# Kernel tuning notes

Hardware: AMD Instinct MI355X
Metric: run time of the kernel (lower is better)

## Reference

```python
import jax, jax.numpy as jnp
import numpy as np

B, T, I = 32768, 28, 28
H, C = 128, 10


def setup_inputs() -> dict:
    key = jax.random.key(0)
    ks = jax.random.split(key, 7)
    s_u = 1.0 / np.sqrt(I)
    s_w = 1.0 / np.sqrt(H)
    return {
        "x": jax.random.normal(ks[0], (B, T, I), dtype=jnp.float32),
        "U_w": jax.random.uniform(ks[1], (H, I), jnp.float32, -s_u, s_u),
        "U_b": jax.random.uniform(ks[2], (H,), jnp.float32, -s_u, s_u),
        "W_w": jax.random.uniform(ks[3], (H, H), jnp.float32, -s_w, s_w),
        "W_b": jax.random.uniform(ks[4], (H,), jnp.float32, -s_w, s_w),
        "V_w": jax.random.uniform(ks[5], (C, H), jnp.float32, -s_w, s_w),
        "V_b": jax.random.uniform(ks[6], (C,), jnp.float32, -s_w, s_w),
    }


def reference(x, U_w, U_b, W_w, W_b, V_w, V_b):
    # x: [B, T, I]. Precompute input projections for all timesteps at once
    # (one big GEMM), then scan the sequential recurrence on S.
    ux = jnp.einsum("bti,hi->tbh", x, U_w) + U_b  # [T, B, H]

    def step(S, ux_t):
        S = jnp.tanh(ux_t + S @ W_w.T + W_b)
        return S, None

    S0 = jnp.zeros((x.shape[0], W_w.shape[0]), dtype=x.dtype)
    S_final, _ = jax.lax.scan(step, S0, ux)
    return S_final @ V_w.T + V_b  # [B, C]
```

## Files before the change

kernel.cpp:

```cpp
#include <hip/hip_runtime.h>


#define T_STEPS 28
#define S_STRIDE 132
#define X_STRIDE 900
#define XSLOTS 3136

typedef __attribute__((ext_vector_type(4))) float f32x4;
typedef __attribute__((ext_vector_type(8))) short short8;

#define MFMA16 __builtin_amdgcn_mfma_f32_16x16x32_bf16

__device__ __forceinline__ unsigned pack2(float lo, float hi) {
#if __has_builtin(__builtin_amdgcn_cvt_pk_bf16_f32)
  auto p = __builtin_amdgcn_cvt_pk_bf16_f32(lo, hi);
  return __builtin_bit_cast(unsigned, p);
#else
  unsigned a = __builtin_bit_cast(unsigned, lo);
  a += 0x7FFFu + ((a >> 16) & 1u);
  unsigned b = __builtin_bit_cast(unsigned, hi);
  b += 0x7FFFu + ((b >> 16) & 1u);
  return (a >> 16) | (b & 0xFFFF0000u);
#endif
}

__device__ __forceinline__ short8 to_frag(f32x4 a, f32x4 b) {
  union { unsigned u[4]; short8 v; } r;
  r.u[0] = pack2(a[0], a[1]);
  r.u[1] = pack2(a[2], a[3]);
  r.u[2] = pack2(b[0], b[1]);
  r.u[3] = pack2(b[2], b[3]);
  return r.v;
}

__device__ __forceinline__ short8 load_frag64(const unsigned short* sp, int off) {
  union { uint2 d[2]; short8 v; } r;
  r.d[0] = *(const uint2*)(sp + off);
  r.d[1] = *(const uint2*)(sp + off + 4);
  return r.v;
}

__device__ __forceinline__ float fast_exp2(float a) {
#if __has_builtin(__builtin_amdgcn_exp2f)
  return __builtin_amdgcn_exp2f(a);
#else
  return __exp2f(a);
#endif
}

__device__ __forceinline__ f32x4 tanh4(f32x4 z) {
  f32x4 t;
#pragma unroll
  for (int i = 0; i < 4; ++i) {
    float e = fast_exp2(z[i] * 2.885390081777927f);
    float r = __builtin_amdgcn_rcpf(1.0f + e);
    t[i] = __builtin_fmaf(r, -2.0f, 1.0f);
  }
  return t;
}

__global__ __launch_bounds__(256, 4) void rnn_fused(
    const float* __restrict__ x,  const float* __restrict__ Uw,
    const float* __restrict__ Ub, const float* __restrict__ Ww,
    const float* __restrict__ Wb, const float* __restrict__ Vw,
    const float* __restrict__ Vb, float* __restrict__ out) {
  __shared__ __align__(16) unsigned short Sbuf[2][16 * S_STRIDE];
  __shared__ __align__(16) unsigned short Xbuf[16 * X_STRIDE];

  const int tid  = threadIdx.x;
  const int w    = tid >> 6;
  const int lane = tid & 63;
  const int l15  = lane & 15;
  const int q    = lane >> 4;
  const int mrow = w * 32;
  const int b0   = blockIdx.x * 16;

  const f32x4 zero4 = {0.f, 0.f, 0.f, 0.f};
  const float* xblk = x + (size_t)b0 * 784;

  {
    f32x4 xr[13];
#pragma unroll
    for (int k = 0; k < 13; ++k) {
      int s = tid + 256 * k;
      if (s < XSLOTS) xr[k] = *(const f32x4*)(xblk + s * 4);
    }
#pragma unroll
    for (int k = 0; k < 13; ++k) {
      int s = tid + 256 * k;
      if (s < XSLOTS) {
        int row = s / 196, g = s - row * 196, tt = g / 7, j = g - tt * 7;
        uint2 d; d.x = pack2(xr[k][0], xr[k][1]); d.y = pack2(xr[k][2], xr[k][3]);
        *(uint2*)(Xbuf + row * X_STRIDE + tt * 32 + j * 4) = d;
        if (j == 0) {
          uint2 zz; zz.x = 0u; zz.y = 0u;
          *(uint2*)(Xbuf + row * X_STRIDE + tt * 32 + 28) = zz;
        }
      }
    }
  }

  short8 wfrag[2][4];
  short8 ufrag[2];
  f32x4  bias[2];
#pragma unroll
  for (int mt = 0; mt < 2; ++mt) {
    const int h = mrow + mt * 16 + l15;
    const float* wp = Ww + h * 128 + q * 8;
#pragma unroll
    for (int kt = 0; kt < 4; ++kt) {
      wfrag[mt][kt] = to_frag(*(const f32x4*)wp, *(const f32x4*)(wp + 4));
      wp += 32;
    }
    const float* up = Uw + h * 28 + q * 8;
    f32x4 u0 = *(const f32x4*)up;
    f32x4 u1 = zero4;
    if (q < 3) u1 = *(const f32x4*)(up + 4);
    ufrag[mt] = to_frag(u0, u1);
    const int hb = mrow + mt * 16 + q * 4;
    bias[mt] = *(const f32x4*)(Wb + hb) + *(const f32x4*)(Ub + hb);
  }
  __syncthreads();

  const int ro = l15 * S_STRIDE;
  const int xo = l15 * X_STRIDE + q * 8;
  f32x4 acc[2];

  {
    short8 xf = load_frag64(&Xbuf[0], xo);
    unsigned short* wp = &Sbuf[1][0];
#pragma unroll
    for (int mt = 0; mt < 2; ++mt) {
      f32x4 d0 = MFMA16(ufrag[mt], xf, bias[mt], 0, 0, 0);
      f32x4 t0 = tanh4(d0);
      uint2 dd; dd.x = pack2(t0[0], t0[1]); dd.y = pack2(t0[2], t0[3]);
      *(uint2*)(wp + ro + mrow + mt * 16 + q * 4) = dd;
    }
  }
  __syncthreads();

#pragma unroll 1
  for (int t = 1; t < T_STEPS; ++t) {
    short8 xf = load_frag64(&Xbuf[0], xo + t * 32);

    const unsigned short* sp = &Sbuf[t & 1][0] + ro + q * 8;

    short8 sA = load_frag64(sp, 0);
#pragma unroll
    for (int mt = 0; mt < 2; ++mt)
      acc[mt] = MFMA16(wfrag[mt][0], sA, bias[mt], 0, 0, 0);
#pragma unroll
    for (int kt = 1; kt < 4; ++kt) {
      sA = load_frag64(sp, kt * 32);
#pragma unroll
      for (int mt = 0; mt < 2; ++mt)
        acc[mt] = MFMA16(wfrag[mt][kt], sA, acc[mt], 0, 0, 0);
    }
#pragma unroll
    for (int mt = 0; mt < 2; ++mt)
      acc[mt] = MFMA16(ufrag[mt], xf, acc[mt], 0, 0, 0);

    unsigned short* wp = &Sbuf[(t + 1) & 1][0];
#pragma unroll
    for (int mt = 0; mt < 2; ++mt) {
      f32x4 th = tanh4(acc[mt]);
      uint2 dd; dd.x = pack2(th[0], th[1]); dd.y = pack2(th[2], th[3]);
      *(uint2*)(wp + ro + mrow + mt * 16 + q * 4) = dd;
    }
    __syncthreads();
  }

  if (w == 0) {
    short8 vfrag[4];
    const float* vp = Vw + l15 * 128 + q * 8;
#pragma unroll
    for (int kt = 0; kt < 4; ++kt) {
      f32x4 v0 = zero4, v1 = zero4;
      if (l15 < 10) {
        v0 = *(const f32x4*)(vp + kt * 32);
        v1 = *(const f32x4*)(vp + kt * 32 + 4);
      }
      vfrag[kt] = to_frag(v0, v1);
    }
    const unsigned short* sp = &Sbuf[0][0] + ro + q * 8;
    f32x4 o;
#pragma unroll
    for (int r = 0; r < 4; ++r) {
      const int c = q * 4 + r;
      o[r] = (c < 10) ? Vb[c] : 0.f;
    }
#pragma unroll
    for (int kt = 0; kt < 4; ++kt)
      o = MFMA16(vfrag[kt], load_frag64(sp, kt * 32), o, 0, 0, 0);
#pragma unroll
    for (int r = 0; r < 4; ++r) {
      const int c = q * 4 + r;
      if (c < 10) out[(size_t)(b0 + l15) * 10 + c] = o[r];
    }
  }
}

extern "C" void kernel_launch(void* const* d_in, const int* in_sizes, int n_in,
                              void* d_out, int out_size, void* d_ws, size_t ws_size,
                              hipStream_t stream) {
  const float* x  = (const float*)d_in[0];
  const float* Uw = (const float*)d_in[1];
  const float* Ub = (const float*)d_in[2];
  const float* Ww = (const float*)d_in[3];
  const float* Wb = (const float*)d_in[4];
  const float* Vw = (const float*)d_in[5];
  const float* Vb = (const float*)d_in[6];
  rnn_fused<<<2048, 256, 0, stream>>>(x, Uw, Ub, Ww, Wb, Vw, Vb, (float*)d_out);
}
```

Measured before the change: 189.7 us.

## Process 32 batch rows per block and stage inputs in time chunks

```diff
diff --git a/kernel.cpp b/kernel.cpp
--- a/kernel.cpp
+++ b/kernel.cpp
@@ -3,8 +3,7 @@
 
 #define T_STEPS 28
 #define S_STRIDE 132
-#define X_STRIDE 900
-#define XSLOTS 3136
+#define X_STRIDE 324
 
 typedef __attribute__((ext_vector_type(4))) float f32x4;
 typedef __attribute__((ext_vector_type(8))) short short8;
@@ -59,13 +58,45 @@
   return t;
 }
 
+template <int NT>
+__device__ __forceinline__ void stage_chunk(const float* __restrict__ xblk,
+                                            unsigned short* __restrict__ Xb,
+                                            int tid, int t0) {
+  constexpr int SLOTS = 32 * NT * 7;
+  constexpr int ITERS = (SLOTS + 255) / 256;
+  f32x4 xr[ITERS];
+#pragma unroll
+  for (int k = 0; k < ITERS; ++k) {
+    const int s = tid + 256 * k;
+    if (s < SLOTS) {
+      const int row = s / (NT * 7), g = s - row * (NT * 7);
+      const int tt = g / 7, j = g - tt * 7;
+      xr[k] = *(const f32x4*)(xblk + row * 784 + (t0 + tt) * 28 + j * 4);
+    }
+  }
+#pragma unroll
+  for (int k = 0; k < ITERS; ++k) {
+    const int s = tid + 256 * k;
+    if (s < SLOTS) {
+      const int row = s / (NT * 7), g = s - row * (NT * 7);
+      const int tt = g / 7, j = g - tt * 7;
+      uint2 d; d.x = pack2(xr[k][0], xr[k][1]); d.y = pack2(xr[k][2], xr[k][3]);
+      *(uint2*)(Xb + row * X_STRIDE + tt * 32 + j * 4) = d;
+      if (j == 0) {
+        uint2 zz; zz.x = 0u; zz.y = 0u;
+        *(uint2*)(Xb + row * X_STRIDE + tt * 32 + 28) = zz;
+      }
+    }
+  }
+}
+
 __global__ __launch_bounds__(256, 4) void rnn_fused(
     const float* __restrict__ x,  const float* __restrict__ Uw,
     const float* __restrict__ Ub, const float* __restrict__ Ww,
     const float* __restrict__ Wb, const float* __restrict__ Vw,
     const float* __restrict__ Vb, float* __restrict__ out) {
-  __shared__ __align__(16) unsigned short Sbuf[2][16 * S_STRIDE];
-  __shared__ __align__(16) unsigned short Xbuf[16 * X_STRIDE];
+  __shared__ __align__(16) unsigned short Sbuf[2][32 * S_STRIDE];
+  __shared__ __align__(16) unsigned short Xbuf[32 * X_STRIDE];
 
   const int tid  = threadIdx.x;
   const int w    = tid >> 6;
@@ -73,32 +104,12 @@
   const int l15  = lane & 15;
   const int q    = lane >> 4;
   const int mrow = w * 32;
-  const int b0   = blockIdx.x * 16;
+  const int b0   = blockIdx.x * 32;
 
   const f32x4 zero4 = {0.f, 0.f, 0.f, 0.f};
   const float* xblk = x + (size_t)b0 * 784;
 
-  {
-    f32x4 xr[13];
-#pragma unroll
-    for (int k = 0; k < 13; ++k) {
-      int s = tid + 256 * k;
-      if (s < XSLOTS) xr[k] = *(const f32x4*)(xblk + s * 4);
-    }
-#pragma unroll
-    for (int k = 0; k < 13; ++k) {
-      int s = tid + 256 * k;
-      if (s < XSLOTS) {
-        int row = s / 196, g = s - row * 196, tt = g / 7, j = g - tt * 7;
-        uint2 d; d.x = pack2(xr[k][0], xr[k][1]); d.y = pack2(xr[k][2], xr[k][3]);
-        *(uint2*)(Xbuf + row * X_STRIDE + tt * 32 + j * 4) = d;
-        if (j == 0) {
-          uint2 zz; zz.x = 0u; zz.y = 0u;
-          *(uint2*)(Xbuf + row * X_STRIDE + tt * 32 + 28) = zz;
-        }
-      }
-    }
-  }
+  stage_chunk<10>(xblk, Xbuf, tid, 0);
 
   short8 wfrag[2][4];
   short8 ufrag[2];
@@ -122,55 +133,86 @@
   }
   __syncthreads();
 
-  const int ro = l15 * S_STRIDE;
-  const int xo = l15 * X_STRIDE + q * 8;
-  f32x4 acc[2];
+  const int ro0 = l15 * S_STRIDE;
+  const int ro1 = (16 + l15) * S_STRIDE;
+  const int xo0 = l15 * X_STRIDE + q * 8;
+  const int xo1 = (16 + l15) * X_STRIDE + q * 8;
+  const int dcol = mrow + q * 4;
+  f32x4 acc[2][2];
+
+  auto step = [&](int t, int tt) {
+    short8 xf0 = load_frag64(&Xbuf[0], xo0 + tt * 32);
+    short8 xf1 = load_frag64(&Xbuf[0], xo1 + tt * 32);
+    const unsigned short* sb = &Sbuf[t & 1][0] + q * 8;
+
+    short8 s0 = load_frag64(sb, ro0);
+    short8 s1 = load_frag64(sb, ro1);
+#pragma unroll
+    for (int mt = 0; mt < 2; ++mt) {
+      acc[mt][0] = MFMA16(wfrag[mt][0], s0, bias[mt], 0, 0, 0);
+      acc[mt][1] = MFMA16(wfrag[mt][0], s1, bias[mt], 0, 0, 0);
+    }
+#pragma unroll
+    for (int kt = 1; kt < 4; ++kt) {
+      s0 = load_frag64(sb, ro0 + kt * 32);
+      s1 = load_frag64(sb, ro1 + kt * 32);
+#pragma unroll
+      for (int mt = 0; mt < 2; ++mt) {
+        acc[mt][0] = MFMA16(wfrag[mt][kt], s0, acc[mt][0], 0, 0, 0);
+        acc[mt][1] = MFMA16(wfrag[mt][kt], s1, acc[mt][1], 0, 0, 0);
+      }
+    }
+#pragma unroll
+    for (int mt = 0; mt < 2; ++mt) {
+      acc[mt][0] = MFMA16(ufrag[mt], xf0, acc[mt][0], 0, 0, 0);
+      acc[mt][1] = MFMA16(ufrag[mt], xf1, acc[mt][1], 0, 0, 0);
+    }
+
+    unsigned short* wp = &Sbuf[(t + 1) & 1][0];
+#pragma unroll
+    for (int mt = 0; mt < 2; ++mt) {
+      f32x4 t0 = tanh4(acc[mt][0]);
+      f32x4 t1 = tanh4(acc[mt][1]);
+      uint2 e0; e0.x = pack2(t0[0], t0[1]); e0.y = pack2(t0[2], t0[3]);
+      uint2 e1; e1.x = pack2(t1[0], t1[1]); e1.y = pack2(t1[2], t1[3]);
+      *(uint2*)(wp + ro0 + dcol + mt * 16) = e0;
+      *(uint2*)(wp + ro1 + dcol + mt * 16) = e1;
+    }
+    __syncthreads();
+  };
 
   {
-    short8 xf = load_frag64(&Xbuf[0], xo);
+    short8 xf0 = load_frag64(&Xbuf[0], xo0);
+    short8 xf1 = load_frag64(&Xbuf[0], xo1);
     unsigned short* wp = &Sbuf[1][0];
 #pragma unroll
     for (int mt = 0; mt < 2; ++mt) {
-      f32x4 d0 = MFMA16(ufrag[mt], xf, bias[mt], 0, 0, 0);
+      f32x4 d0 = MFMA16(ufrag[mt], xf0, bias[mt], 0, 0, 0);
+      f32x4 d1 = MFMA16(ufrag[mt], xf1, bias[mt], 0, 0, 0);
       f32x4 t0 = tanh4(d0);
-      uint2 dd; dd.x = pack2(t0[0], t0[1]); dd.y = pack2(t0[2], t0[3]);
-      *(uint2*)(wp + ro + mrow + mt * 16 + q * 4) = dd;
+      f32x4 t1 = tanh4(d1);
+      uint2 e0; e0.x = pack2(t0[0], t0[1]); e0.y = pack2(t0[2], t0[3]);
+      uint2 e1; e1.x = pack2(t1[0], t1[1]); e1.y = pack2(t1[2], t1[3]);
+      *(uint2*)(wp + ro0 + dcol + mt * 16) = e0;
+      *(uint2*)(wp + ro1 + dcol + mt * 16) = e1;
     }
   }
   __syncthreads();
 
 #pragma unroll 1
-  for (int t = 1; t < T_STEPS; ++t) {
-    short8 xf = load_frag64(&Xbuf[0], xo + t * 32);
-
-    const unsigned short* sp = &Sbuf[t & 1][0] + ro + q * 8;
-
-    short8 sA = load_frag64(sp, 0);
-#pragma unroll
-    for (int mt = 0; mt < 2; ++mt)
-      acc[mt] = MFMA16(wfrag[mt][0], sA, bias[mt], 0, 0, 0);
-#pragma unroll
-    for (int kt = 1; kt < 4; ++kt) {
-      sA = load_frag64(sp, kt * 32);
-#pragma unroll
-      for (int mt = 0; mt < 2; ++mt)
-        acc[mt] = MFMA16(wfrag[mt][kt], sA, acc[mt], 0, 0, 0);
-    }
-#pragma unroll
-    for (int mt = 0; mt < 2; ++mt)
-      acc[mt] = MFMA16(ufrag[mt], xf, acc[mt], 0, 0, 0);
-
-    unsigned short* wp = &Sbuf[(t + 1) & 1][0];
-#pragma unroll
-    for (int mt = 0; mt < 2; ++mt) {
-      f32x4 th = tanh4(acc[mt]);
-      uint2 dd; dd.x = pack2(th[0], th[1]); dd.y = pack2(th[2], th[3]);
-      *(uint2*)(wp + ro + mrow + mt * 16 + q * 4) = dd;
-    }
-    __syncthreads();
-  }
-
-  if (w == 0) {
+  for (int t = 1; t < 10; ++t) step(t, t);
+
+  stage_chunk<10>(xblk, Xbuf, tid, 10);
+  __syncthreads();
+#pragma unroll 1
+  for (int t = 10; t < 20; ++t) step(t, t - 10);
+
+  stage_chunk<8>(xblk, Xbuf, tid, 20);
+  __syncthreads();
+#pragma unroll 1
+  for (int t = 20; t < T_STEPS; ++t) step(t, t - 20);
+
+  if (w < 2) {
     short8 vfrag[4];
     const float* vp = Vw + l15 * 128 + q * 8;
 #pragma unroll
@@ -182,7 +224,7 @@
       }
       vfrag[kt] = to_frag(v0, v1);
     }
-    const unsigned short* sp = &Sbuf[0][0] + ro + q * 8;
+    const unsigned short* sp = &Sbuf[0][0] + (w * 16 + l15) * S_STRIDE + q * 8;
     f32x4 o;
 #pragma unroll
     for (int r = 0; r < 4; ++r) {
@@ -195,7 +237,7 @@
 #pragma unroll
     for (int r = 0; r < 4; ++r) {
       const int c = q * 4 + r;
-      if (c < 10) out[(size_t)(b0 + l15) * 10 + c] = o[r];
+      if (c < 10) out[(size_t)(b0 + w * 16 + l15) * 10 + c] = o[r];
     }
   }
 }
@@ -210,5 +252,5 @@
   const float* Wb = (const float*)d_in[4];
   const float* Vw = (const float*)d_in[5];
   const float* Vb = (const float*)d_in[6];
-  rnn_fused<<<2048, 256, 0, stream>>>(x, Uw, Ub, Ww, Wb, Vw, Vb, (float*)d_out);
-}
+  rnn_fused<<<1024, 256, 0, stream>>>(x, Uw, Ub, Ww, Wb, Vw, Vb, (float*)d_out);
+}
```

After: 197.0 us. 3.8% more time.
